# Kernel optimization log

Measured on AMD Instinct MI355X. Metric: run time of the kernel, lower is better.

The kernel has to match this reference:

```python
import jax, jax.numpy as jnp
import numpy as np

SEQ_LEN = 4096
EMBED_DIM = 1024
NUM_HEADS = 16  # head_dim = 64


def setup_inputs() -> dict:
    key = jax.random.key(0)
    k0, k1, k2 = jax.random.split(key, 3)
    std = 0.02
    x = jax.random.normal(k0, (SEQ_LEN, EMBED_DIM), dtype=jnp.float32)
    # torch Linear convention: weight [out_features, in_features], y = x @ W.T + b
    W_qkv = jax.random.normal(k1, (3 * EMBED_DIM, EMBED_DIM), dtype=jnp.float32) * std
    b_qkv = jnp.zeros((3 * EMBED_DIM,), dtype=jnp.float32)
    W_out = jax.random.normal(k2, (EMBED_DIM, EMBED_DIM), dtype=jnp.float32) * std
    b_out = jnp.zeros((EMBED_DIM,), dtype=jnp.float32)
    return {"input": x, "W_qkv": W_qkv, "b_qkv": b_qkv, "W_out": W_out, "b_out": b_out}


def reference(input, W_qkv, b_qkv, W_out, b_out):
    S, E = input.shape
    H = NUM_HEADS
    Dh = E // H
    # fused QKV projection: [S, 3E]
    projected = input @ W_qkv.T + b_qkv
    q, k, v = jnp.split(projected, 3, axis=1)          # each [S, E]
    q = q.reshape(S, H, Dh)
    k = k.reshape(S, H, Dh)
    v = v.reshape(S, H, Dh)
    # unscaled attention (the original applies no 1/sqrt(d) scaling)
    scores = jnp.einsum('shd,thd->hst', q, k)          # [H, S, S] -- full matrix in HBM
    probs = jax.nn.softmax(scores, axis=-1)
    out = jnp.einsum('hst,thd->shd', probs, v)         # [S, H, Dh]
    out = out.reshape(S, E)
    return out @ W_out.T + b_out
```

## Files before the change

### kernel.cpp

```cpp
#include <hip/hip_runtime.h>

typedef unsigned short u16;
typedef short    bf16x8 __attribute__((ext_vector_type(8)));
typedef u16      u16x8  __attribute__((ext_vector_type(8)));
typedef u16      u16x4  __attribute__((ext_vector_type(4)));
typedef float    f32x4  __attribute__((ext_vector_type(4)));
typedef unsigned u32x2  __attribute__((ext_vector_type(2)));

__device__ __forceinline__ u16 f2bf(float f) {
  unsigned x = __float_as_uint(f);
  unsigned r = x + 0x7fffu + ((x >> 16) & 1u);
  return (u16)(r >> 16);
}
__device__ __forceinline__ float bf2f(u16 u) {
  return __uint_as_float(((unsigned)u) << 16);
}
__device__ __forceinline__ float exp2v(float x) {
  float r;
  asm("v_exp_f32 %0, %1" : "=v"(r) : "v"(x));
  return r;
}

__global__ __launch_bounds__(256) void cast_bf16(const float* __restrict__ src,
                                                 u16* __restrict__ dst) {
  int i = blockIdx.x * 256 + threadIdx.x;
  f32x4 v = ((const f32x4*)src)[i];
  u16x4 o;
  o[0] = f2bf(v[0]); o[1] = f2bf(v[1]); o[2] = f2bf(v[2]); o[3] = f2bf(v[3]);
  ((u16x4*)dst)[i] = o;
}

template<int N, int K, bool OUTF32, bool SCALEQ>
__global__ __launch_bounds__(256) void gemm_bt(const u16* __restrict__ A,
                                               const u16* __restrict__ B,
                                               const float* __restrict__ bias,
                                               void* __restrict__ Cout) {
  __shared__ __align__(16) u16 As[2][128 * 32];
  __shared__ __align__(16) u16 Bs[2][128 * 32];
  const int tid = threadIdx.x;
  const int m0 = blockIdx.y * 128, n0 = blockIdx.x * 128;
  const int wave = tid >> 6, lane = tid & 63;
  const int c = lane & 15, g = lane >> 4;
  const int wm = (wave >> 1) * 64, wn = (wave & 1) * 64;
  f32x4 acc[4][4] = {};

  const int sr = wave * 16 + (lane >> 2);
  const int sc = (lane & 3) * 8;

  auto stage = [&](int buf, int k0) {
#pragma unroll
    for (int j = 0; j < 2; j++) {
      __builtin_amdgcn_global_load_lds(
        (const __attribute__((address_space(1))) void*)(A + (size_t)(m0 + j * 64 + sr) * K + k0 + sc),
        (__attribute__((address_space(3))) void*)&As[buf][(j * 64 + wave * 16) * 32], 16, 0, 0);
      __builtin_amdgcn_global_load_lds(
        (const __attribute__((address_space(1))) void*)(B + (size_t)(n0 + j * 64 + sr) * K + k0 + sc),
        (__attribute__((address_space(3))) void*)&Bs[buf][(j * 64 + wave * 16) * 32], 16, 0, 0);
    }
  };

  stage(0, 0);
  __syncthreads();

  const int nT = K / 32;
  for (int t = 0; t < nT; ++t) {
    const int buf = t & 1;
    if (t + 1 < nT) stage(buf ^ 1, (t + 1) * 32);
    bf16x8 af[4], bfr[4];
#pragma unroll
    for (int m = 0; m < 4; m++) af[m]  = *(const bf16x8*)&As[buf][(wm + m * 16 + c) * 32 + g * 8];
#pragma unroll
    for (int n = 0; n < 4; n++) bfr[n] = *(const bf16x8*)&Bs[buf][(wn + n * 16 + c) * 32 + g * 8];
#pragma unroll
    for (int m = 0; m < 4; m++)
#pragma unroll
      for (int n = 0; n < 4; n++)
        acc[m][n] = __builtin_amdgcn_mfma_f32_16x16x32_bf16(af[m], bfr[n], acc[m][n], 0, 0, 0);
    __syncthreads();
  }

  const float qscale = (SCALEQ && n0 < 1024) ? 1.44269504f : 1.0f;
#pragma unroll
  for (int n = 0; n < 4; n++) {
    float bv = bias[n0 + wn + n * 16 + c];
#pragma unroll
    for (int m = 0; m < 4; m++) {
#pragma unroll
      for (int r = 0; r < 4; r++) {
        float val = (acc[m][n][r] + bv) * qscale;
        int row = m0 + wm + m * 16 + g * 4 + r;
        int col = n0 + wn + n * 16 + c;
        if constexpr (OUTF32) ((float*)Cout)[(size_t)row * N + col] = val;
        else                  ((u16*)Cout)[(size_t)row * N + col] = f2bf(val);
      }
    }
  }
}

__global__ __launch_bounds__(256) void transpose_v(const u16* __restrict__ qkv,
                                                   u16* __restrict__ vt) {
  __shared__ u16 tile[64][64];
  int h  = blockIdx.x >> 6;
  int s0 = (blockIdx.x & 63) * 64;
  int t = threadIdx.x;
  int row = t >> 3, ch = t & 7;
#pragma unroll
  for (int rep = 0; rep < 2; rep++) {
    int r = rep * 32 + row;
    u16x8 v = *(const u16x8*)&qkv[(size_t)(s0 + r) * 3072 + 2048 + h * 64 + ch * 8];
    *(u16x8*)&tile[r][ch * 8] = v;
  }
  __syncthreads();
#pragma unroll
  for (int rep = 0; rep < 2; rep++) {
    int d = rep * 32 + row;
    u16x8 w;
#pragma unroll
    for (int j = 0; j < 8; j++) w[j] = tile[ch * 8 + j][d];
    *(u16x8*)&vt[(size_t)(h * 64 + d) * 4096 + s0 + ch * 8] = w;
  }
}

__global__ __launch_bounds__(256, 3) void attn_kernel(const u16* __restrict__ qkv,
                                                      const u16* __restrict__ vt,
                                                      u16* __restrict__ pb0,
                                                      u16* __restrict__ pb1,
                                                      float* __restrict__ lb0,
                                                      float* __restrict__ lb1) {
  const int bid = blockIdx.x;
  const int kk  = bid & 1;
  const int qt  = (bid >> 1) & 31;
  const int h   = bid >> 6;
  const int q0  = qt * 128;
  const int kbase = kk * 2048;
  const int tid = threadIdx.x;
  const int wave = tid >> 6, lane = tid & 63;
  const int c = lane & 15, g = lane >> 4;
  const int qw = q0 + wave * 32;

  __shared__ __align__(16) u16 kls[2][64 * 64];
  __shared__ __align__(16) u16 vls[2][64 * 64];
  __shared__ __align__(16) unsigned plds[4][32 * 36];
  unsigned* pw = plds[wave];

  const u16* Kg = qkv + 1024 + h * 64;
  const u16* Vg = vt + (size_t)h * 64 * 4096;

  const int srow = lane >> 3, sgr = lane & 7;
  const int gc = sgr ^ (srow & 7);
  const u16* kp = Kg + (size_t)(kbase + wave * 16 + srow) * 3072 + gc * 8;
  const u16* vp = Vg + (size_t)(wave * 16 + srow) * 4096 + kbase + gc * 8;

  auto stage = [&](int buf, const u16* kpp, const u16* vpp) {
#pragma unroll
    for (int j = 0; j < 2; j++) {
      __builtin_amdgcn_global_load_lds(
        (const __attribute__((address_space(1))) void*)(kpp + (size_t)j * 8 * 3072),
        (__attribute__((address_space(3))) void*)&kls[buf][(wave * 16 + j * 8) * 64], 16, 0, 0);
      __builtin_amdgcn_global_load_lds(
        (const __attribute__((address_space(1))) void*)(vpp + (size_t)j * 8 * 4096),
        (__attribute__((address_space(3))) void*)&vls[buf][(wave * 16 + j * 8) * 64], 16, 0, 0);
    }
  };

  bf16x8 qf[2][2];
#pragma unroll
  for (int qs = 0; qs < 2; qs++)
#pragma unroll
    for (int dc = 0; dc < 2; dc++)
      qf[qs][dc] = *(const bf16x8*)&qkv[(size_t)(qw + qs * 16 + c) * 3072 + h * 64 + dc * 32 + g * 8];

  bf16x8 ones;
#pragma unroll
  for (int j = 0; j < 8; j++) ones[j] = (short)0x3F80;

  f32x4 o0[4] = {}, o1[4] = {};
  f32x4 accl0 = {}, accl1 = {};
  const f32x4 minit = {-16.f, -16.f, -16.f, -16.f};

  auto softmax = [&](int qs, f32x4 (&st)[4]) {
    unsigned base = (unsigned)(qs * 16 + c) * 36 + g * 2;
#pragma unroll
    for (int ks = 0; ks < 4; ks++) {
      float p0 = exp2v(st[ks][0]), p1 = exp2v(st[ks][1]);
      float p2 = exp2v(st[ks][2]), p3 = exp2v(st[ks][3]);
      unsigned w0, w1;
      asm("v_cvt_pk_bf16_f32 %0, %1, %2" : "=v"(w0) : "v"(p0), "v"(p1));
      asm("v_cvt_pk_bf16_f32 %0, %1, %2" : "=v"(w1) : "v"(p2), "v"(p3));
      u32x2 w2 = {w0, w1};
      *(u32x2*)&pw[base + ks * 8] = w2;
    }
  };

  stage(0, kp, vp);
  kp += (size_t)64 * 3072; vp += 64;
  __syncthreads();

  for (int t = 0; t < 32; ++t) {
    const int buf = t & 1;
    if (t + 1 < 32) {
      stage(buf ^ 1, kp, vp);
      kp += (size_t)64 * 3072; vp += 64;
    }

    {
      f32x4 st[4];
      __builtin_amdgcn_s_setprio(1);
#pragma unroll
      for (int ks = 0; ks < 4; ks++) {
        bf16x8 kf0 = *(const bf16x8*)&kls[buf][(ks * 16 + c) * 64 + ((g ^ (c & 7)) << 3)];
        bf16x8 kf1 = *(const bf16x8*)&kls[buf][(ks * 16 + c) * 64 + (((4 + g) ^ (c & 7)) << 3)];
        f32x4 s = __builtin_amdgcn_mfma_f32_16x16x32_bf16(kf0, qf[0][0], minit, 0, 0, 0);
        st[ks]  = __builtin_amdgcn_mfma_f32_16x16x32_bf16(kf1, qf[0][1], s, 0, 0, 0);
      }
      __builtin_amdgcn_s_setprio(0);
      softmax(0, st);
    }
    {
      f32x4 st[4];
      __builtin_amdgcn_s_setprio(1);
#pragma unroll
      for (int ks = 0; ks < 4; ks++) {
        bf16x8 kf0 = *(const bf16x8*)&kls[buf][(ks * 16 + c) * 64 + ((g ^ (c & 7)) << 3)];
        bf16x8 kf1 = *(const bf16x8*)&kls[buf][(ks * 16 + c) * 64 + (((4 + g) ^ (c & 7)) << 3)];
        f32x4 s = __builtin_amdgcn_mfma_f32_16x16x32_bf16(kf0, qf[1][0], minit, 0, 0, 0);
        st[ks]  = __builtin_amdgcn_mfma_f32_16x16x32_bf16(kf1, qf[1][1], s, 0, 0, 0);
      }
      __builtin_amdgcn_s_setprio(0);
      softmax(1, st);
    }

    bf16x8 pa0[2], pa1[2];
#pragma unroll
    for (int hh = 0; hh < 2; hh++) {
      pa0[hh] = *(const bf16x8*)&pw[(0 * 16 + c) * 36 + hh * 16 + g * 4];
      pa1[hh] = *(const bf16x8*)&pw[(1 * 16 + c) * 36 + hh * 16 + g * 4];
    }

    __builtin_amdgcn_s_setprio(1);
#pragma unroll
    for (int k2 = 0; k2 < 2; k2++) {
      accl0 = __builtin_amdgcn_mfma_f32_16x16x32_bf16(pa0[k2], ones, accl0, 0, 0, 0);
      accl1 = __builtin_amdgcn_mfma_f32_16x16x32_bf16(pa1[k2], ones, accl1, 0, 0, 0);
#pragma unroll
      for (int dt = 0; dt < 4; dt++) {
        bf16x8 vf = *(const bf16x8*)&vls[buf][(dt * 16 + c) * 64 + (((k2 * 4 + g) ^ (c & 7)) << 3)];
        o0[dt] = __builtin_amdgcn_mfma_f32_16x16x32_bf16(pa0[k2], vf, o0[dt], 0, 0, 0);
        o1[dt] = __builtin_amdgcn_mfma_f32_16x16x32_bf16(pa1[k2], vf, o1[dt], 0, 0, 0);
      }
    }
    __builtin_amdgcn_s_setprio(0);
    __syncthreads();
  }

  u16* pb = kk ? pb1 : pb0;
  float* lb = (kk ? lb1 : lb0) + h * 4096 + qw;
  u16* pq = pb + (size_t)qw * 1024 + h * 64;

#pragma unroll
  for (int r = 0; r < 4; r++) {
    int rl = g * 4 + r;
    float inv0 = 1.0f / accl0[r];
    float inv1 = 1.0f / accl1[r];
#pragma unroll
    for (int dt = 0; dt < 4; dt++) {
      pq[(size_t)rl * 1024 + dt * 16 + c]        = f2bf(o0[dt][r] * inv0);
      pq[(size_t)(16 + rl) * 1024 + dt * 16 + c] = f2bf(o1[dt][r] * inv1);
    }
    if (c == 0) {
      lb[rl]      = accl0[r];
      lb[16 + rl] = accl1[r];
    }
  }
}

__global__ __launch_bounds__(256) void combine_kernel(u16* __restrict__ pb0,
                                                      const u16* __restrict__ pb1,
                                                      const float* __restrict__ lb0,
                                                      const float* __restrict__ lb1) {
  int t = blockIdx.x * 256 + threadIdx.x;
  int q = t >> 7;
  int c8 = t & 127;
  int h = c8 >> 3;
  float A = lb0[h * 4096 + q];
  float B = lb1[h * 4096 + q];
  float inv = 1.0f / (A + B);
  float w0 = A * inv, w1 = B * inv;
  size_t off = (size_t)q * 1024 + c8 * 8;
  u16x8 x0 = *(const u16x8*)(pb0 + off);
  u16x8 x1 = *(const u16x8*)(pb1 + off);
  u16x8 o;
#pragma unroll
  for (int e = 0; e < 8; e++)
    o[e] = f2bf(bf2f(x0[e]) * w0 + bf2f(x1[e]) * w1);
  *(u16x8*)(pb0 + off) = o;
}

extern "C" void kernel_launch(void* const* d_in, const int* in_sizes, int n_in,
                              void* d_out, int out_size, void* d_ws, size_t ws_size,
                              hipStream_t stream) {
  const float* x    = (const float*)d_in[0];
  const float* Wqkv = (const float*)d_in[1];
  const float* bqkv = (const float*)d_in[2];
  const float* Wout = (const float*)d_in[3];
  const float* bout = (const float*)d_in[4];

  char* ws = (char*)d_ws;
  u16* xb    = (u16*)(ws);
  u16* wqkvb = (u16*)(ws + (size_t)8  * (1u << 20));
  u16* woutb = (u16*)(ws + (size_t)14 * (1u << 20));
  u16* qkvb  = (u16*)(ws + (size_t)16 * (1u << 20));
  u16* vtb   = (u16*)(ws + (size_t)40 * (1u << 20));
  u16* pb0   = (u16*)(ws + (size_t)48 * (1u << 20));
  char* dob = (char*)d_out;
  u16*   pb1 = (u16*)dob;
  float* lb0 = (float*)(dob + (size_t)8 * (1u << 20));
  float* lb1 = lb0 + 65536;

  cast_bf16<<<4096, 256, 0, stream>>>(x,    xb);
  cast_bf16<<<3072, 256, 0, stream>>>(Wqkv, wqkvb);
  cast_bf16<<<1024, 256, 0, stream>>>(Wout, woutb);

  gemm_bt<3072, 1024, false, true><<<dim3(24, 32), 256, 0, stream>>>(xb, wqkvb, bqkv, qkvb);

  transpose_v<<<1024, 256, 0, stream>>>(qkvb, vtb);

  attn_kernel<<<1024, 256, 0, stream>>>(qkvb, vtb, pb0, pb1, lb0, lb1);

  combine_kernel<<<2048, 256, 0, stream>>>(pb0, pb1, lb0, lb1);

  gemm_bt<1024, 1024, true, false><<<dim3(8, 32), 256, 0, stream>>>(pb0, woutb, bout, d_out);
}
```

Before: 186.1 us.

## Shrink per-wave P scratch with XOR swizzle, raise attention occupancy, swizzle GEMM blocks

The attention kernel now uses a per-wave P staging buffer half the previous size (16 rows instead of 32). It uses an XOR swizzle in place of padding, and reuses the buffer for the two query sub-tiles one after the other. All QK^T MFMAs for both sub-tiles are interleaved in one loop. Together with the smaller LDS footprint, this lets launch bounds request 4 blocks per CU instead of 3. The GEMM also remaps block indices in strides of eight for better L2 locality. The changes risk register pressure at the higher occupancy and add serialization between the two softmax/read phases.

```diff
diff --git a/kernel.cpp b/kernel.cpp
--- a/kernel.cpp
+++ b/kernel.cpp
@@ -38,7 +38,10 @@
   __shared__ __align__(16) u16 As[2][128 * 32];
   __shared__ __align__(16) u16 Bs[2][128 * 32];
   const int tid = threadIdx.x;
-  const int m0 = blockIdx.y * 128, n0 = blockIdx.x * 128;
+  const int flat = blockIdx.y * gridDim.x + blockIdx.x;
+  const int q8 = (gridDim.x * gridDim.y) >> 3;
+  const int sw = (flat & 7) * q8 + (flat >> 3);
+  const int m0 = (sw / gridDim.x) * 128, n0 = (sw % gridDim.x) * 128;
   const int wave = tid >> 6, lane = tid & 63;
   const int c = lane & 15, g = lane >> 4;
   const int wm = (wave >> 1) * 64, wn = (wave & 1) * 64;
@@ -121,7 +124,7 @@
   }
 }
 
-__global__ __launch_bounds__(256, 3) void attn_kernel(const u16* __restrict__ qkv,
+__global__ __launch_bounds__(256, 4) void attn_kernel(const u16* __restrict__ qkv,
                                                       const u16* __restrict__ vt,
                                                       u16* __restrict__ pb0,
                                                       u16* __restrict__ pb1,
@@ -140,8 +143,9 @@
 
   __shared__ __align__(16) u16 kls[2][64 * 64];
   __shared__ __align__(16) u16 vls[2][64 * 64];
-  __shared__ __align__(16) unsigned plds[4][32 * 36];
+  __shared__ __align__(16) unsigned plds[4][16 * 32];
   unsigned* pw = plds[wave];
+  const int pswz = (c & 7) << 2;
 
   const u16* Kg = qkv + 1024 + h * 64;
   const u16* Vg = vt + (size_t)h * 64 * 4096;
@@ -178,8 +182,7 @@
   f32x4 accl0 = {}, accl1 = {};
   const f32x4 minit = {-16.f, -16.f, -16.f, -16.f};
 
-  auto softmax = [&](int qs, f32x4 (&st)[4]) {
-    unsigned base = (unsigned)(qs * 16 + c) * 36 + g * 2;
+  auto softmax = [&](f32x4 (&st)[4]) {
 #pragma unroll
     for (int ks = 0; ks < 4; ks++) {
       float p0 = exp2v(st[ks][0]), p1 = exp2v(st[ks][1]);
@@ -188,7 +191,7 @@
       asm("v_cvt_pk_bf16_f32 %0, %1, %2" : "=v"(w0) : "v"(p0), "v"(p1));
       asm("v_cvt_pk_bf16_f32 %0, %1, %2" : "=v"(w1) : "v"(p2), "v"(p3));
       u32x2 w2 = {w0, w1};
-      *(u32x2*)&pw[base + ks * 8] = w2;
+      *(u32x2*)&pw[c * 32 + ((ks * 8 + g * 2) ^ pswz)] = w2;
     }
   };
 
@@ -203,39 +206,28 @@
       kp += (size_t)64 * 3072; vp += 64;
     }
 
-    {
-      f32x4 st[4];
-      __builtin_amdgcn_s_setprio(1);
-#pragma unroll
-      for (int ks = 0; ks < 4; ks++) {
-        bf16x8 kf0 = *(const bf16x8*)&kls[buf][(ks * 16 + c) * 64 + ((g ^ (c & 7)) << 3)];
-        bf16x8 kf1 = *(const bf16x8*)&kls[buf][(ks * 16 + c) * 64 + (((4 + g) ^ (c & 7)) << 3)];
-        f32x4 s = __builtin_amdgcn_mfma_f32_16x16x32_bf16(kf0, qf[0][0], minit, 0, 0, 0);
-        st[ks]  = __builtin_amdgcn_mfma_f32_16x16x32_bf16(kf1, qf[0][1], s, 0, 0, 0);
-      }
-      __builtin_amdgcn_s_setprio(0);
-      softmax(0, st);
-    }
-    {
-      f32x4 st[4];
-      __builtin_amdgcn_s_setprio(1);
-#pragma unroll
-      for (int ks = 0; ks < 4; ks++) {
-        bf16x8 kf0 = *(const bf16x8*)&kls[buf][(ks * 16 + c) * 64 + ((g ^ (c & 7)) << 3)];
-        bf16x8 kf1 = *(const bf16x8*)&kls[buf][(ks * 16 + c) * 64 + (((4 + g) ^ (c & 7)) << 3)];
-        f32x4 s = __builtin_amdgcn_mfma_f32_16x16x32_bf16(kf0, qf[1][0], minit, 0, 0, 0);
-        st[ks]  = __builtin_amdgcn_mfma_f32_16x16x32_bf16(kf1, qf[1][1], s, 0, 0, 0);
-      }
-      __builtin_amdgcn_s_setprio(0);
-      softmax(1, st);
-    }
-
+    f32x4 st0[4], st1[4];
+    __builtin_amdgcn_s_setprio(1);
+#pragma unroll
+    for (int ks = 0; ks < 4; ks++) {
+      bf16x8 kf0 = *(const bf16x8*)&kls[buf][(ks * 16 + c) * 64 + ((g ^ (c & 7)) << 3)];
+      bf16x8 kf1 = *(const bf16x8*)&kls[buf][(ks * 16 + c) * 64 + (((4 + g) ^ (c & 7)) << 3)];
+      f32x4 s0 = __builtin_amdgcn_mfma_f32_16x16x32_bf16(kf0, qf[0][0], minit, 0, 0, 0);
+      st0[ks]  = __builtin_amdgcn_mfma_f32_16x16x32_bf16(kf1, qf[0][1], s0, 0, 0, 0);
+      f32x4 s1 = __builtin_amdgcn_mfma_f32_16x16x32_bf16(kf0, qf[1][0], minit, 0, 0, 0);
+      st1[ks]  = __builtin_amdgcn_mfma_f32_16x16x32_bf16(kf1, qf[1][1], s1, 0, 0, 0);
+    }
+    __builtin_amdgcn_s_setprio(0);
+
+    softmax(st0);
     bf16x8 pa0[2], pa1[2];
 #pragma unroll
-    for (int hh = 0; hh < 2; hh++) {
-      pa0[hh] = *(const bf16x8*)&pw[(0 * 16 + c) * 36 + hh * 16 + g * 4];
-      pa1[hh] = *(const bf16x8*)&pw[(1 * 16 + c) * 36 + hh * 16 + g * 4];
-    }
+    for (int hh = 0; hh < 2; hh++)
+      pa0[hh] = *(const bf16x8*)&pw[c * 32 + ((hh * 16 + g * 4) ^ pswz)];
+    softmax(st1);
+#pragma unroll
+    for (int hh = 0; hh < 2; hh++)
+      pa1[hh] = *(const bf16x8*)&pw[c * 32 + ((hh * 16 + g * 4) ^ pswz)];
 
     __builtin_amdgcn_s_setprio(1);
 #pragma unroll
```

Result: faster. 176.8 us (-5.0%).
